# Kernel optimization log

Measured on AMD Instinct MI355X. Metric: run time of the kernel, lower is better.

The kernel has to match this reference:

```python
import jax, jax.numpy as jnp
import numpy as np

C = 64          # channels
K = 15          # sum(shell_sizes)=1+14
H = 32          # neighbors per query
N = 50000       # support points (== query points M)
RADIUS = 1.0
SIGMA = 0.7
INF = 1e6
BN_EPS = 1e-5


def _init_kernel_points(key):
    # stand-in for load_kernels: 1 center point + 14 points on a sphere shell
    pts = jax.random.normal(key, (K - 1, 3), dtype=jnp.float32)
    pts = pts / jnp.linalg.norm(pts, axis=1, keepdims=True) * RADIUS
    return jnp.concatenate([jnp.zeros((1, 3), jnp.float32), pts], axis=0)


def setup_inputs() -> dict:
    key = jax.random.key(0)
    ks = jax.random.split(key, 10)
    q_pts = jax.random.normal(ks[0], (N, 3), dtype=jnp.float32)
    s_pts = jax.random.normal(ks[1], (N, 3), dtype=jnp.float32)
    s_feats = jax.random.normal(ks[2], (N, C), dtype=jnp.float32)
    neighb_inds = jax.random.randint(ks[3], (N, H), 0, N)
    kernel_points = _init_kernel_points(ks[4])
    # alpha_mlp: Linear(C->C, no bias) -> BatchNorm -> LeakyReLU(0.1) -> Linear(C->K*C)
    lim1 = 1.0 / np.sqrt(C)
    W1 = jax.random.uniform(ks[5], (C, C), jnp.float32, -lim1, lim1)
    gamma = jnp.ones((C,), jnp.float32)
    beta = jnp.zeros((C,), jnp.float32)
    W2 = jax.random.uniform(ks[6], (C, K * C), jnp.float32, -lim1, lim1)
    b2 = jax.random.uniform(ks[7], (K * C,), jnp.float32, -lim1, lim1)
    return {"q_pts": q_pts, "s_pts": s_pts, "s_feats": s_feats,
            "neighb_inds": neighb_inds, "kernel_points": kernel_points,
            "W1": W1, "gamma": gamma, "beta": beta, "W2": W2, "b2": b2}


def reference(q_pts, s_pts, s_feats, neighb_inds, kernel_points, W1, gamma, beta, W2, b2):
    M = q_pts.shape[0]
    # alpha_mlp on pooled (= center) features: (M, C) -> (M, K*C)
    h = s_feats @ W1
    mu = jnp.mean(h, axis=0)
    var = jnp.var(h, axis=0)
    h = (h - mu) / jnp.sqrt(var + BN_EPS) * gamma + beta
    h = jax.nn.leaky_relu(h, 0.1)
    conv_weights = (h @ W2 + b2).reshape(M, K, C)

    # gather neighbor features with a zero padding row (index N -> zeros)
    padded_feats = jnp.concatenate([s_feats, jnp.zeros((1, C), s_feats.dtype)], axis=0)
    neighbor_feats = padded_feats[neighb_inds]                 # (M, H, C)

    # relative neighbor positions with inf padding point
    s_pts_pad = jnp.concatenate([s_pts, jnp.full((1, 3), INF, s_pts.dtype)], axis=0)
    neighbors = s_pts_pad[neighb_inds] - q_pts[:, None, :]     # (M, H, 3)

    # kernel-point influence: nearest kernel point + linear influence
    diff = neighbors[:, :, None, :] - kernel_points            # (M, H, K, 3)
    sq_d = jnp.sum(diff * diff, axis=-1)                       # (M, H, K)
    nn_sq = jnp.min(sq_d, axis=-1)                             # (M, H)
    nn_idx = jnp.argmin(sq_d, axis=-1)                         # (M, H)
    infl = jnp.clip(1.0 - jnp.sqrt(nn_sq) / SIGMA, 0.0)        # (M, H)

    # per-neighbor channel weights from the MLP output, gathered by 1nn kernel point
    nw = jnp.take_along_axis(conv_weights, nn_idx[:, :, None], axis=1)  # (M, H, C)
    nw = nw * infl[:, :, None]

    # weighted aggregation (merge=mul, aggr=sum over neighbors)
    return jnp.sum(neighbor_feats * nw, axis=1)                # (M, C)
```

## Files before the change

### kernel.cpp

```cpp
#include <hip/hip_runtime.h>
#include <math.h>

#define N_PTS 50000
#define CCH   64
#define KP    15
#define NH    32
#define SIGMA 0.7f
#define BN_EPS 1e-5f
#define LEAKY 0.1f
#define QB    32
#define NBLK  ((N_PTS + QB - 1) / QB)
#define STATS_BLOCKS 1024
#define SP4_BLOCKS 196
#define CW_KSTRIDE_B 4224

typedef short bf16x8 __attribute__((ext_vector_type(8)));
typedef float floatx4 __attribute__((ext_vector_type(4)));

__device__ __forceinline__ unsigned short f2b(float f) {
    union { float f; unsigned u; } v; v.f = f;
    return (unsigned short)((v.u + 0x7FFFu + ((v.u >> 16) & 1u)) >> 16);
}
__device__ __forceinline__ float b2f(unsigned short b) {
    union { unsigned u; float f; } v; v.u = ((unsigned)b) << 16;
    return v.f;
}
__device__ __forceinline__ float blo(unsigned u) {
    union { unsigned u; float f; } v; v.u = u << 16;
    return v.f;
}
__device__ __forceinline__ float bhi(unsigned u) {
    union { unsigned u; float f; } v; v.u = u & 0xFFFF0000u;
    return v.f;
}
__device__ __forceinline__ unsigned cvtpk(float lo, float hi) {
    unsigned r;
    asm("v_cvt_pk_bf16_f32 %0, %1, %2" : "=v"(r) : "v"(lo), "v"(hi));
    return r;
}

__global__ __launch_bounds__(256) void k_prep(const float* __restrict__ sf,
                                              const float* __restrict__ W1,
                                              const float* __restrict__ W2,
                                              const float* __restrict__ s_pts,
                                              const float* __restrict__ kpts,
                                              float* __restrict__ bn,
                                              unsigned short* __restrict__ hst,
                                              unsigned short* __restrict__ w2b,
                                              unsigned short* __restrict__ sfb,
                                              float* __restrict__ sp4,
                                              float* __restrict__ kpc4) {
    int t = threadIdx.x;
    if (blockIdx.x >= STATS_BLOCKS + 30 + SP4_BLOCKS) {
        if (t < KP) {
            float x = kpts[t * 3 + 0], y = kpts[t * 3 + 1], z = kpts[t * 3 + 2];
            float4 v; v.x = x; v.y = y; v.z = z; v.w = 0.5f * (x * x + y * y + z * z);
            *(float4*)(kpc4 + t * 4) = v;
        }
        return;
    }
    if (blockIdx.x >= STATS_BLOCKS + 30) {
        int g = (blockIdx.x - STATS_BLOCKS - 30) * 256 + t;
        if (g < N_PTS) {
            float4 v;
            v.x = s_pts[g * 3 + 0]; v.y = s_pts[g * 3 + 1];
            v.z = s_pts[g * 3 + 2]; v.w = 0.f;
            *(float4*)(sp4 + g * 4) = v;
        }
        return;
    }
    if (blockIdx.x >= STATS_BLOCKS) {
        int g = (blockIdx.x - STATS_BLOCKS) * 256 + t;
        int lane = g & 63, s = (g >> 6) & 1, tt = g >> 7;
        int col = lane & 15, quad = lane >> 4;
        int base = (s * 32 + quad * 8) * 960 + tt * 16 + col;
        ushort4 lo, hi;
        lo.x = f2b(W2[base + 0 * 960]); lo.y = f2b(W2[base + 1 * 960]);
        lo.z = f2b(W2[base + 2 * 960]); lo.w = f2b(W2[base + 3 * 960]);
        hi.x = f2b(W2[base + 4 * 960]); hi.y = f2b(W2[base + 5 * 960]);
        hi.z = f2b(W2[base + 6 * 960]); hi.w = f2b(W2[base + 7 * 960]);
        *(ushort4*)(w2b + g * 8)     = lo;
        *(ushort4*)(w2b + g * 8 + 4) = hi;
        return;
    }
    int c = t & 63, ml = t >> 6;
    float w1c[64];
    #pragma unroll
    for (int i = 0; i < 64; ++i) w1c[i] = W1[i * 64 + c];
    __shared__ float rows[16][64];
    float acc_s = 0.f, acc_q = 0.f;
    for (int tile = blockIdx.x; tile < N_PTS / 16; tile += STATS_BLOCKS) {
        int m0 = tile * 16;
        __syncthreads();
        float4 v = *(const float4*)(sf + m0 * 64 + t * 4);
        ((float4*)rows)[t] = v;
        ushort4 s4;
        s4.x = f2b(v.x); s4.y = f2b(v.y); s4.z = f2b(v.z); s4.w = f2b(v.w);
        *(ushort4*)(sfb + m0 * 64 + t * 4) = s4;
        __syncthreads();
        #pragma unroll
        for (int rr = 0; rr < 4; ++rr) {
            int r = ml + rr * 4;
            float h = 0.f;
            #pragma unroll
            for (int i4 = 0; i4 < 16; ++i4) {
                float4 rv = *(const float4*)&rows[r][i4 * 4];
                h += rv.x * w1c[i4 * 4] + rv.y * w1c[i4 * 4 + 1]
                   + rv.z * w1c[i4 * 4 + 2] + rv.w * w1c[i4 * 4 + 3];
            }
            acc_s += h;
            acc_q += h * h;
            hst[(m0 + r) * 64 + c] = f2b(h);
        }
    }
    __shared__ float red[2][256];
    red[0][t] = acc_s; red[1][t] = acc_q;
    __syncthreads();
    if (t < 64) {
        float s = red[0][t] + red[0][64 + t] + red[0][128 + t] + red[0][192 + t];
        float q = red[1][t] + red[1][64 + t] + red[1][128 + t] + red[1][192 + t];
        atomicAdd(&bn[t], s);
        atomicAdd(&bn[64 + t], q);
    }
}

__global__ __launch_bounds__(256, 2) void k_main(
    const float* __restrict__ q_pts, const float* __restrict__ sp4,
    const unsigned short* __restrict__ sfb, const int* __restrict__ nb,
    const float* __restrict__ kpc4, const float* __restrict__ gamma,
    const float* __restrict__ beta, const float* __restrict__ bn,
    const float* __restrict__ b2, const unsigned short* __restrict__ w2b,
    const unsigned short* __restrict__ hst, float* __restrict__ out) {

    __shared__ __align__(16) unsigned cwP[KP * 32 * 33];
    __shared__ float abS[128];
    __shared__ int      nCnt[QB];
    __shared__ unsigned nPack[QB][NH];
    __shared__ float    nInf[QB][NH];

    int t = threadIdx.x;
    int lane = t & 63, wv = t >> 6;
    int m0 = blockIdx.x * QB;

    int qb = t >> 5, hh = t & 31;
    int mq0 = min(m0 + qb,      N_PTS - 1);
    int mq1 = min(m0 + qb + 8,  N_PTS - 1);
    int mq2 = min(m0 + qb + 16, N_PTS - 1);
    int mq3 = min(m0 + qb + 24, N_PTS - 1);
    int idx0 = nb[mq0 * NH + hh];
    int idx1 = nb[mq1 * NH + hh];
    int idx2 = nb[mq2 * NH + hh];
    int idx3 = nb[mq3 * NH + hh];

    if (t < 64) {
        float mu  = bn[t] * (1.0f / N_PTS);
        float var = bn[64 + t] * (1.0f / N_PTS) - mu * mu;
        float a   = gamma[t] * rsqrtf(var + BN_EPS);
        abS[t]      = a;
        abS[64 + t] = beta[t] - mu * a;
    }

    int row = lane & 15, half = lane >> 4;
    bf16x8 r0, r1, r0b, r1b;
    {
        int ra = min(m0 + row,      N_PTS - 1);
        int rb = min(m0 + 16 + row, N_PTS - 1);
        const unsigned short* ha = hst + ra * 64 + half * 8;
        const unsigned short* hb = hst + rb * 64 + half * 8;
        r0  = *(const bf16x8*)(ha);        r1  = *(const bf16x8*)(ha + 32);
        r0b = *(const bf16x8*)(hb);        r1b = *(const bf16x8*)(hb + 32);
    }

    float4 sp0 = *(const float4*)(sp4 + idx0 * 4);
    float4 sp1 = *(const float4*)(sp4 + idx1 * 4);
    float4 sp2 = *(const float4*)(sp4 + idx2 * 4);
    float4 sp3 = *(const float4*)(sp4 + idx3 * 4);
    float qx0 = q_pts[mq0 * 3 + 0], qy0 = q_pts[mq0 * 3 + 1], qz0 = q_pts[mq0 * 3 + 2];
    float qx1 = q_pts[mq1 * 3 + 0], qy1 = q_pts[mq1 * 3 + 1], qz1 = q_pts[mq1 * 3 + 2];
    float qx2 = q_pts[mq2 * 3 + 0], qy2 = q_pts[mq2 * 3 + 1], qz2 = q_pts[mq2 * 3 + 2];
    float qx3 = q_pts[mq3 * 3 + 0], qy3 = q_pts[mq3 * 3 + 1], qz3 = q_pts[mq3 * 3 + 2];

    float4 kq[KP];
    #pragma unroll
    for (int i = 0; i < KP; ++i) kq[i] = *(const float4*)(kpc4 + i * 4);

    __syncthreads();

    unsigned pf0 = 0, pf1 = 0, pf2 = 0, pf3 = 0, pf4 = 0, pf5 = 0, pf6 = 0, pf7 = 0;
#define PHASE1(SP, QX, QY, QZ, IDX, QOFF, PFA, PFB)                                   \
    {                                                                                 \
        int q = qb + QOFF;                                                            \
        float px = SP.x - QX, py = SP.y - QY, pz = SP.z - QZ;                         \
        float pn = px * px + py * py + pz * pz;                                       \
        float best = 1e30f; int bi = 0;                                               \
        _Pragma("unroll")                                                             \
        for (int k = 0; k < KP; ++k) {                                                \
            float val = kq[k].w - (px * kq[k].x + py * kq[k].y + pz * kq[k].z);       \
            if (val < best) { best = val; bi = k; }                                   \
        }                                                                             \
        float d2 = fmaxf(fmaf(2.f, best, pn), 0.f);                                   \
        float infl = 1.f - sqrtf(d2) * (1.0f / SIGMA);                                \
        bool keep = infl > 0.f;                                                       \
        unsigned long long bal = __ballot(keep);                                      \
        unsigned mym = (unsigned)(bal >> (lane & 32));                                \
        unsigned below = mym & ((1u << (lane & 31)) - 1u);                            \
        int cnt = __popc(mym);                                                        \
        int pos = keep ? __popc(below) : cnt + ((lane & 31) - __popc(below));         \
        nPack[q][pos] = keep ? ((unsigned)IDX | ((unsigned)(bi * CW_KSTRIDE_B) << 16)) \
                             : 0u;                                                    \
        nInf[q][pos]  = keep ? infl : 0.f;                                            \
        if (keep) {                                                                   \
            const unsigned* rowp = (const unsigned*)(sfb + IDX * 64);                 \
            PFA = rowp[0]; PFB = rowp[16];                                            \
        }                                                                             \
        if ((lane & 31) == 0) nCnt[q] = cnt;                                          \
    }
    PHASE1(sp0, qx0, qy0, qz0, idx0, 0,  pf0, pf1)
    PHASE1(sp1, qx1, qy1, qz1, idx1, 8,  pf2, pf3)
    PHASE1(sp2, qx2, qy2, qz2, idx2, 16, pf4, pf5)
    PHASE1(sp3, qx3, qy3, qz3, idx3, 24, pf6, pf7)
#undef PHASE1

    bf16x8 a0, a1, a0b, a1b;
    {
        unsigned* A0 = (unsigned*)&a0;  unsigned* A1 = (unsigned*)&a1;
        unsigned* B0 = (unsigned*)&a0b; unsigned* B1 = (unsigned*)&a1b;
        #pragma unroll
        for (int jw = 0; jw < 4; ++jw) {
            int c0 = half * 8 + jw * 2;
            int c1 = 32 + c0;
            float g00 = abS[c0]     * b2f((unsigned short)r0[jw * 2])     + abS[64 + c0];
            float g01 = abS[c0 + 1] * b2f((unsigned short)r0[jw * 2 + 1]) + abS[64 + c0 + 1];
            A0[jw] = cvtpk(fmaxf(g00, LEAKY * g00), fmaxf(g01, LEAKY * g01));
            float g10 = abS[c1]     * b2f((unsigned short)r1[jw * 2])     + abS[64 + c1];
            float g11 = abS[c1 + 1] * b2f((unsigned short)r1[jw * 2 + 1]) + abS[64 + c1 + 1];
            A1[jw] = cvtpk(fmaxf(g10, LEAKY * g10), fmaxf(g11, LEAKY * g11));
            float h00 = abS[c0]     * b2f((unsigned short)r0b[jw * 2])     + abS[64 + c0];
            float h01 = abS[c0 + 1] * b2f((unsigned short)r0b[jw * 2 + 1]) + abS[64 + c0 + 1];
            B0[jw] = cvtpk(fmaxf(h00, LEAKY * h00), fmaxf(h01, LEAKY * h01));
            float h10 = abS[c1]     * b2f((unsigned short)r1b[jw * 2])     + abS[64 + c1];
            float h11 = abS[c1 + 1] * b2f((unsigned short)r1b[jw * 2 + 1]) + abS[64 + c1 + 1];
            B1[jw] = cvtpk(fmaxf(h10, LEAKY * h10), fmaxf(h11, LEAKY * h11));
        }
    }

    {
        int colq = lane & 15, quad = lane >> 4;
        bf16x8 Lf[3], Ls[3], Mf[3], Ms[3];
        #pragma unroll
        for (int i = 0; i < 3; ++i) {
            int tt = wv * 15 + i;
            Lf[i] = *(const bf16x8*)(w2b + ((tt * 2 + 0) * 64 + lane) * 8);
            Ls[i] = *(const bf16x8*)(w2b + ((tt * 2 + 1) * 64 + lane) * 8);
        }
        #pragma unroll
        for (int g = 0; g < 5; ++g) {
            if (g < 4) {
                #pragma unroll
                for (int i = 0; i < 3; ++i) {
                    int tt = wv * 15 + (g + 1) * 3 + i;
                    Mf[i] = *(const bf16x8*)(w2b + ((tt * 2 + 0) * 64 + lane) * 8);
                    Ms[i] = *(const bf16x8*)(w2b + ((tt * 2 + 1) * 64 + lane) * 8);
                }
            }
            #pragma unroll
            for (int i = 0; i < 3; ++i) {
                int tt = wv * 15 + g * 3 + i;
                floatx4 accA = {0.f, 0.f, 0.f, 0.f};
                floatx4 accB = {0.f, 0.f, 0.f, 0.f};
                accA = __builtin_amdgcn_mfma_f32_16x16x32_bf16(Lf[i], a0,  accA, 0, 0, 0);
                accA = __builtin_amdgcn_mfma_f32_16x16x32_bf16(Ls[i], a1,  accA, 0, 0, 0);
                accB = __builtin_amdgcn_mfma_f32_16x16x32_bf16(Lf[i], a0b, accB, 0, 0, 0);
                accB = __builtin_amdgcn_mfma_f32_16x16x32_bf16(Ls[i], a1b, accB, 0, 0, 0);
                int n0 = tt * 16 + quad * 4;
                float4 bb = *(const float4*)&b2[n0];
                int k  = n0 >> 6;
                int c2 = (n0 & 63) >> 1;
                unsigned w0 = cvtpk(accA[0] + bb.x, accA[1] + bb.y);
                unsigned w1 = cvtpk(accA[2] + bb.z, accA[3] + bb.w);
                unsigned w2 = cvtpk(accB[0] + bb.x, accB[1] + bb.y);
                unsigned w3 = cvtpk(accB[2] + bb.z, accB[3] + bb.w);
                unsigned* dst = cwP + (k * 1056 + c2 * 33 + colq);
                dst[0]  = w0;
                dst[33] = w1;
                dst[16] = w2;
                dst[49] = w3;
            }
            if (g < 4) {
                #pragma unroll
                for (int i = 0; i < 3; ++i) { Lf[i] = Mf[i]; Ls[i] = Ms[i]; }
            }
        }
    }
    asm volatile("" :: "v"(pf0), "v"(pf1), "v"(pf2), "v"(pf3),
                       "v"(pf4), "v"(pf5), "v"(pf6), "v"(pf7));
    __syncthreads();

    {
        int r = lane >> 5, c2 = lane & 31;
        const unsigned short* sfbC = sfb + c2 * 2;
        const unsigned char* cwB = (const unsigned char*)cwP;
        #pragma unroll
        for (int pp = 0; pp < 4; ++pp) {
            int qa = wv * 8 + pp * 2;
            int q  = qa + r;
            const unsigned* packRow = &nPack[q][0];
            const float*    infRow  = &nInf[q][0];
            const unsigned char* cwLane = cwB + (c2 * 33 + q) * 4;
            int nA = nCnt[qa], nB = nCnt[qa + 1];
            int na = nA > nB ? nA : nB;
            float acc0 = 0.f, acc1 = 0.f;
            for (int jj = 0; jj < na; jj += 4) {
                uint4  pk = *(const uint4*)&packRow[jj];
                float4 in = *(const float4*)&infRow[jj];
                unsigned f0 = *(const unsigned*)(sfbC + (pk.x & 0xFFFFu) * 64);
                unsigned f1 = *(const unsigned*)(sfbC + (pk.y & 0xFFFFu) * 64);
                unsigned f2 = *(const unsigned*)(sfbC + (pk.z & 0xFFFFu) * 64);
                unsigned f3 = *(const unsigned*)(sfbC + (pk.w & 0xFFFFu) * 64);
                unsigned w0 = *(const unsigned*)(cwLane + (pk.x >> 16));
                unsigned w1 = *(const unsigned*)(cwLane + (pk.y >> 16));
                unsigned w2 = *(const unsigned*)(cwLane + (pk.z >> 16));
                unsigned w3 = *(const unsigned*)(cwLane + (pk.w >> 16));
                acc0 = fmaf(in.x * blo(f0), blo(w0), acc0);
                acc1 = fmaf(in.x * bhi(f0), bhi(w0), acc1);
                acc0 = fmaf(in.y * blo(f1), blo(w1), acc0);
                acc1 = fmaf(in.y * bhi(f1), bhi(w1), acc1);
                acc0 = fmaf(in.z * blo(f2), blo(w2), acc0);
                acc1 = fmaf(in.z * bhi(f2), bhi(w2), acc1);
                acc0 = fmaf(in.w * blo(f3), blo(w3), acc0);
                acc1 = fmaf(in.w * bhi(f3), bhi(w3), acc1);
            }
            if (m0 + q < N_PTS) {
                float2 o; o.x = acc0; o.y = acc1;
                *(float2*)&out[(m0 + q) * 64 + c2 * 2] = o;
            }
        }
    }
}

extern "C" void kernel_launch(void* const* d_in, const int* in_sizes, int n_in,
                              void* d_out, int out_size, void* d_ws, size_t ws_size,
                              hipStream_t stream) {
    const float* q_pts   = (const float*)d_in[0];
    const float* s_pts   = (const float*)d_in[1];
    const float* s_feats = (const float*)d_in[2];
    const int*   nb      = (const int*)d_in[3];
    const float* kpts    = (const float*)d_in[4];
    const float* W1      = (const float*)d_in[5];
    const float* gamma   = (const float*)d_in[6];
    const float* beta    = (const float*)d_in[7];
    const float* W2      = (const float*)d_in[8];
    const float* b2      = (const float*)d_in[9];
    float* out = (float*)d_out;

    float* ws = (float*)d_ws;
    float* bn = ws;
    unsigned short* w2b = (unsigned short*)(ws + 128);
    unsigned short* hst = w2b + 61440;
    unsigned short* sfb = hst + N_PTS * CCH;
    float* sp4 = (float*)(sfb + N_PTS * CCH);
    float* kpc4 = sp4 + N_PTS * 4;

    hipMemsetAsync(bn, 0, 128 * sizeof(float), stream);
    k_prep<<<STATS_BLOCKS + 30 + SP4_BLOCKS + 1, 256, 0, stream>>>(
        s_feats, W1, W2, s_pts, kpts, bn, hst, w2b, sfb, sp4, kpc4);
    k_main<<<NBLK, 256, 0, stream>>>(q_pts, sp4, sfb, nb, kpc4,
                                     gamma, beta, bn, b2, w2b, hst, out);
}
```

Before: 159.0 us.

## Halve conv-weight LDS tile by processing queries in two halves

The per-block conv-weight tile in shared memory is halved. The second 16 queries' MFMA results are held in registers (st0/st1) and written to LDS only after the first half's aggregation finishes, with extra barriers between the halves. Influence values are stored as fp16 instead of fp32, and launch bounds request 4 blocks per CU instead of 2, aiming for higher occupancy to hide gather latency. The costs are extra synchronisation, 30 more live registers per thread, a less prefetch-friendly W2 load loop, and slightly lower precision on influence weights.

```diff
diff --git a/kernel.cpp b/kernel.cpp
--- a/kernel.cpp
+++ b/kernel.cpp
@@ -1,4 +1,5 @@
 #include <hip/hip_runtime.h>
+#include <hip/hip_fp16.h>
 #include <math.h>
 
 #define N_PTS 50000
@@ -12,7 +13,7 @@
 #define NBLK  ((N_PTS + QB - 1) / QB)
 #define STATS_BLOCKS 1024
 #define SP4_BLOCKS 196
-#define CW_KSTRIDE_B 4224
+#define CW_KSTRIDE_B 2176
 
 typedef short bf16x8 __attribute__((ext_vector_type(8)));
 typedef float floatx4 __attribute__((ext_vector_type(4)));
@@ -37,6 +38,14 @@
     unsigned r;
     asm("v_cvt_pk_bf16_f32 %0, %1, %2" : "=v"(r) : "v"(lo), "v"(hi));
     return r;
+}
+__device__ __forceinline__ unsigned short f2h(float f) {
+    __half h = __float2half(f);
+    return *reinterpret_cast<unsigned short*>(&h);
+}
+__device__ __forceinline__ float h2f(unsigned short b) {
+    __half h = *reinterpret_cast<__half*>(&b);
+    return __half2float(h);
 }
 
 __global__ __launch_bounds__(256) void k_prep(const float* __restrict__ sf,
@@ -124,7 +133,7 @@
     }
 }
 
-__global__ __launch_bounds__(256, 2) void k_main(
+__global__ __launch_bounds__(256, 4) void k_main(
     const float* __restrict__ q_pts, const float* __restrict__ sp4,
     const unsigned short* __restrict__ sfb, const int* __restrict__ nb,
     const float* __restrict__ kpc4, const float* __restrict__ gamma,
@@ -132,11 +141,11 @@
     const float* __restrict__ b2, const unsigned short* __restrict__ w2b,
     const unsigned short* __restrict__ hst, float* __restrict__ out) {
 
-    __shared__ __align__(16) unsigned cwP[KP * 32 * 33];
+    __shared__ __align__(16) unsigned cwP[KP * 32 * 17];
     __shared__ float abS[128];
-    __shared__ int      nCnt[QB];
-    __shared__ unsigned nPack[QB][NH];
-    __shared__ float    nInf[QB][NH];
+    __shared__ int            nCnt[QB];
+    __shared__ unsigned       nPack[QB][NH];
+    __shared__ unsigned short nInfH[QB][NH];
 
     int t = threadIdx.x;
     int lane = t & 63, wv = t >> 6;
@@ -208,7 +217,7 @@
         int pos = keep ? __popc(below) : cnt + ((lane & 31) - __popc(below));         \
         nPack[q][pos] = keep ? ((unsigned)IDX | ((unsigned)(bi * CW_KSTRIDE_B) << 16)) \
                              : 0u;                                                    \
-        nInf[q][pos]  = keep ? infl : 0.f;                                            \
+        nInfH[q][pos] = keep ? f2h(infl) : (unsigned short)0;                         \
         if (keep) {                                                                   \
             const unsigned* rowp = (const unsigned*)(sfb + IDX * 64);                 \
             PFA = rowp[0]; PFB = rowp[16];                                            \
@@ -244,98 +253,97 @@
         }
     }
 
+    unsigned st0[15], st1[15];
+    int colq = lane & 15, quad = lane >> 4;
     {
-        int colq = lane & 15, quad = lane >> 4;
-        bf16x8 Lf[3], Ls[3], Mf[3], Ms[3];
         #pragma unroll
-        for (int i = 0; i < 3; ++i) {
+        for (int i = 0; i < 15; ++i) {
             int tt = wv * 15 + i;
-            Lf[i] = *(const bf16x8*)(w2b + ((tt * 2 + 0) * 64 + lane) * 8);
-            Ls[i] = *(const bf16x8*)(w2b + ((tt * 2 + 1) * 64 + lane) * 8);
-        }
-        #pragma unroll
-        for (int g = 0; g < 5; ++g) {
-            if (g < 4) {
-                #pragma unroll
-                for (int i = 0; i < 3; ++i) {
-                    int tt = wv * 15 + (g + 1) * 3 + i;
-                    Mf[i] = *(const bf16x8*)(w2b + ((tt * 2 + 0) * 64 + lane) * 8);
-                    Ms[i] = *(const bf16x8*)(w2b + ((tt * 2 + 1) * 64 + lane) * 8);
-                }
-            }
-            #pragma unroll
-            for (int i = 0; i < 3; ++i) {
-                int tt = wv * 15 + g * 3 + i;
-                floatx4 accA = {0.f, 0.f, 0.f, 0.f};
-                floatx4 accB = {0.f, 0.f, 0.f, 0.f};
-                accA = __builtin_amdgcn_mfma_f32_16x16x32_bf16(Lf[i], a0,  accA, 0, 0, 0);
-                accA = __builtin_amdgcn_mfma_f32_16x16x32_bf16(Ls[i], a1,  accA, 0, 0, 0);
-                accB = __builtin_amdgcn_mfma_f32_16x16x32_bf16(Lf[i], a0b, accB, 0, 0, 0);
-                accB = __builtin_amdgcn_mfma_f32_16x16x32_bf16(Ls[i], a1b, accB, 0, 0, 0);
-                int n0 = tt * 16 + quad * 4;
-                float4 bb = *(const float4*)&b2[n0];
-                int k  = n0 >> 6;
-                int c2 = (n0 & 63) >> 1;
-                unsigned w0 = cvtpk(accA[0] + bb.x, accA[1] + bb.y);
-                unsigned w1 = cvtpk(accA[2] + bb.z, accA[3] + bb.w);
-                unsigned w2 = cvtpk(accB[0] + bb.x, accB[1] + bb.y);
-                unsigned w3 = cvtpk(accB[2] + bb.z, accB[3] + bb.w);
-                unsigned* dst = cwP + (k * 1056 + c2 * 33 + colq);
-                dst[0]  = w0;
-                dst[33] = w1;
-                dst[16] = w2;
-                dst[49] = w3;
-            }
-            if (g < 4) {
-                #pragma unroll
-                for (int i = 0; i < 3; ++i) { Lf[i] = Mf[i]; Ls[i] = Ms[i]; }
-            }
+            bf16x8 f0 = *(const bf16x8*)(w2b + ((tt * 2 + 0) * 64 + lane) * 8);
+            bf16x8 f1 = *(const bf16x8*)(w2b + ((tt * 2 + 1) * 64 + lane) * 8);
+            floatx4 accA = {0.f, 0.f, 0.f, 0.f};
+            floatx4 accB = {0.f, 0.f, 0.f, 0.f};
+            accA = __builtin_amdgcn_mfma_f32_16x16x32_bf16(f0, a0,  accA, 0, 0, 0);
+            accA = __builtin_amdgcn_mfma_f32_16x16x32_bf16(f1, a1,  accA, 0, 0, 0);
+            accB = __builtin_amdgcn_mfma_f32_16x16x32_bf16(f0, a0b, accB, 0, 0, 0);
+            accB = __builtin_amdgcn_mfma_f32_16x16x32_bf16(f1, a1b, accB, 0, 0, 0);
+            int n0 = tt * 16 + quad * 4;
+            float4 bb = *(const float4*)&b2[n0];
+            int k  = n0 >> 6;
+            int c2 = (n0 & 63) >> 1;
+            unsigned* dst = cwP + (k * 544 + c2 * 17 + colq);
+            dst[0]  = cvtpk(accA[0] + bb.x, accA[1] + bb.y);
+            dst[17] = cvtpk(accA[2] + bb.z, accA[3] + bb.w);
+            st0[i]  = cvtpk(accB[0] + bb.x, accB[1] + bb.y);
+            st1[i]  = cvtpk(accB[2] + bb.z, accB[3] + bb.w);
         }
     }
     asm volatile("" :: "v"(pf0), "v"(pf1), "v"(pf2), "v"(pf3),
                        "v"(pf4), "v"(pf5), "v"(pf6), "v"(pf7));
     __syncthreads();
 
+    int r = lane >> 5, c2 = lane & 31;
+    const unsigned short* sfbC = sfb + c2 * 2;
+    const unsigned char* cwB = (const unsigned char*)cwP;
+#define PHASEB(QGRP)                                                                  \
+    {                                                                                 \
+        _Pragma("unroll")                                                             \
+        for (int pp = 0; pp < 2; ++pp) {                                              \
+            int qa = wv * 4 + pp * 2;                    \
+            int qc = qa + r;                                                          \
+            int Q  = QGRP * 16 + qc;                       \
+            const unsigned*       packRow = &nPack[Q][0];                             \
+            const unsigned short* infRow  = &nInfH[Q][0];                             \
+            const unsigned char* cwLane = cwB + (c2 * 17 + qc) * 4;                   \
+            int nA = nCnt[QGRP * 16 + qa], nB = nCnt[QGRP * 16 + qa + 1];             \
+            int na = nA > nB ? nA : nB;                                               \
+            float acc0 = 0.f, acc1 = 0.f;                                             \
+            for (int jj = 0; jj < na; jj += 4) {                                      \
+                uint4   pk = *(const uint4*)&packRow[jj];      \
+                ushort4 ih = *(const ushort4*)&infRow[jj];                            \
+                float i0 = h2f(ih.x), i1 = h2f(ih.y), i2 = h2f(ih.z), i3 = h2f(ih.w); \
+                unsigned f0 = *(const unsigned*)(sfbC + (pk.x & 0xFFFFu) * 64);       \
+                unsigned f1 = *(const unsigned*)(sfbC + (pk.y & 0xFFFFu) * 64);       \
+                unsigned f2 = *(const unsigned*)(sfbC + (pk.z & 0xFFFFu) * 64);       \
+                unsigned f3 = *(const unsigned*)(sfbC + (pk.w & 0xFFFFu) * 64);       \
+                unsigned w0 = *(const unsigned*)(cwLane + (pk.x >> 16));              \
+                unsigned w1 = *(const unsigned*)(cwLane + (pk.y >> 16));              \
+                unsigned w2 = *(const unsigned*)(cwLane + (pk.z >> 16));              \
+                unsigned w3 = *(const unsigned*)(cwLane + (pk.w >> 16));              \
+                acc0 = fmaf(i0 * blo(f0), blo(w0), acc0);                             \
+                acc1 = fmaf(i0 * bhi(f0), bhi(w0), acc1);                             \
+                acc0 = fmaf(i1 * blo(f1), blo(w1), acc0);                             \
+                acc1 = fmaf(i1 * bhi(f1), bhi(w1), acc1);                             \
+                acc0 = fmaf(i2 * blo(f2), blo(w2), acc0);                             \
+                acc1 = fmaf(i2 * bhi(f2), bhi(w2), acc1);                             \
+                acc0 = fmaf(i3 * blo(f3), blo(w3), acc0);                             \
+                acc1 = fmaf(i3 * bhi(f3), bhi(w3), acc1);                             \
+            }                                                                         \
+            if (m0 + Q < N_PTS) {                                                     \
+                float2 o; o.x = acc0; o.y = acc1;                                     \
+                *(float2*)&out[(m0 + Q) * 64 + c2 * 2] = o;                           \
+            }                                                                         \
+        }                                                                             \
+    }
+    PHASEB(0)
+
+    __syncthreads();
     {
-        int r = lane >> 5, c2 = lane & 31;
-        const unsigned short* sfbC = sfb + c2 * 2;
-        const unsigned char* cwB = (const unsigned char*)cwP;
         #pragma unroll
-        for (int pp = 0; pp < 4; ++pp) {
-            int qa = wv * 8 + pp * 2;
-            int q  = qa + r;
-            const unsigned* packRow = &nPack[q][0];
-            const float*    infRow  = &nInf[q][0];
-            const unsigned char* cwLane = cwB + (c2 * 33 + q) * 4;
-            int nA = nCnt[qa], nB = nCnt[qa + 1];
-            int na = nA > nB ? nA : nB;
-            float acc0 = 0.f, acc1 = 0.f;
-            for (int jj = 0; jj < na; jj += 4) {
-                uint4  pk = *(const uint4*)&packRow[jj];
-                float4 in = *(const float4*)&infRow[jj];
-                unsigned f0 = *(const unsigned*)(sfbC + (pk.x & 0xFFFFu) * 64);
-                unsigned f1 = *(const unsigned*)(sfbC + (pk.y & 0xFFFFu) * 64);
-                unsigned f2 = *(const unsigned*)(sfbC + (pk.z & 0xFFFFu) * 64);
-                unsigned f3 = *(const unsigned*)(sfbC + (pk.w & 0xFFFFu) * 64);
-                unsigned w0 = *(const unsigned*)(cwLane + (pk.x >> 16));
-                unsigned w1 = *(const unsigned*)(cwLane + (pk.y >> 16));
-                unsigned w2 = *(const unsigned*)(cwLane + (pk.z >> 16));
-                unsigned w3 = *(const unsigned*)(cwLane + (pk.w >> 16));
-                acc0 = fmaf(in.x * blo(f0), blo(w0), acc0);
-                acc1 = fmaf(in.x * bhi(f0), bhi(w0), acc1);
-                acc0 = fmaf(in.y * blo(f1), blo(w1), acc0);
-                acc1 = fmaf(in.y * bhi(f1), bhi(w1), acc1);
-                acc0 = fmaf(in.z * blo(f2), blo(w2), acc0);
-                acc1 = fmaf(in.z * bhi(f2), bhi(w2), acc1);
-                acc0 = fmaf(in.w * blo(f3), blo(w3), acc0);
-                acc1 = fmaf(in.w * bhi(f3), bhi(w3), acc1);
-            }
-            if (m0 + q < N_PTS) {
-                float2 o; o.x = acc0; o.y = acc1;
-                *(float2*)&out[(m0 + q) * 64 + c2 * 2] = o;
-            }
-        }
-    }
+        for (int i = 0; i < 15; ++i) {
+            int tt = wv * 15 + i;
+            int n0 = tt * 16 + quad * 4;
+            int k  = n0 >> 6;
+            int cc = (n0 & 63) >> 1;
+            unsigned* dst = cwP + (k * 544 + cc * 17 + colq);
+            dst[0]  = st0[i];
+            dst[17] = st1[i];
+        }
+    }
+    __syncthreads();
+
+    PHASEB(1)
+#undef PHASEB
 }
 
 extern "C" void kernel_launch(void* const* d_in, const int* in_sizes, int n_in,
```

After: 155.6 us. 2.2% less time.
